# Performance work log

Hardware: AMD Instinct MI355X
Metric: run time of the kernel (lower is better)

The kernel has to match this reference:

```python
import jax, jax.numpy as jnp
import numpy as np

B, S, C, HEADS, DMODEL = 16, 14, 2048, 4, 512
C8 = C // 8
N = S * S
F = C * N  # flattened per-head feature size


def setup_inputs() -> dict:
    key = jax.random.key(0)
    ks = jax.random.split(key, 12)
    scale = 0.02
    return {
        "encoded_before_images": jax.random.normal(ks[0], (B, S, S, C), jnp.float32),
        "encoded_after_images": jax.random.normal(ks[1], (B, S, S, C), jnp.float32),
        "Wq": jax.random.normal(ks[2], (HEADS, C8, C), jnp.float32) * scale,
        "bq": jax.random.normal(ks[3], (HEADS, C8), jnp.float32) * scale,
        "Wk": jax.random.normal(ks[4], (HEADS, C8, C), jnp.float32) * scale,
        "bk": jax.random.normal(ks[5], (HEADS, C8), jnp.float32) * scale,
        "Wv": jax.random.normal(ks[6], (HEADS, C, C), jnp.float32) * scale,
        "bv": jax.random.normal(ks[7], (HEADS, C), jnp.float32) * scale,
        "gamma": jax.random.normal(ks[8], (HEADS,), jnp.float32) * 0.1,
        "Wl": jax.random.normal(ks[9], (DMODEL, F), jnp.float32) * 0.005,
        "bl": jax.random.normal(ks[10], (DMODEL,), jnp.float32) * scale,
    }


def reference(encoded_before_images, encoded_after_images,
              Wq, bq, Wk, bk, Wv, bv, gamma, Wl, bl):
    # permute to (B, C, H, W) then flatten spatial -> (B, C, N)
    before = jnp.transpose(encoded_before_images, (0, 3, 1, 2)).reshape(B, C, N)
    after = jnp.transpose(encoded_after_images, (0, 3, 1, 2)).reshape(B, C, N)
    diff = (after - before) / (HEADS - 1)
    i = jnp.arange(HEADS, dtype=before.dtype)[:, None, None, None]
    x = before[None] + i * diff[None]        # image_trajectory: (H, B, C, N)
    d = i * diff[None]                        # change_trajectory: (H, B, C, N)

    # per-head 1x1 convs (Q from image, K from change image, V from image)
    Q = jnp.einsum('hoc,hbcn->hbno', Wq, x) + bq[:, None, None, :]   # (H,B,N,C8)
    K = jnp.einsum('hoc,hbcn->hbon', Wk, d) + bk[:, None, :, None]   # (H,B,C8,N)
    energy = jnp.einsum('hbno,hbom->hbnm', Q, K)                     # (H,B,N,N)
    attn = jax.nn.softmax(energy, axis=-1)
    V = jnp.einsum('hoc,hbcn->hbon', Wv, x) + bv[:, None, :, None]   # (H,B,C,N)
    # out[b,c,m] = sum_n V[b,c,n] * attn[b,m,n]
    out = jnp.einsum('hbcn,hbmn->hbcm', V, attn)                      # (H,B,C,N)
    out = gamma[:, None, None, None] * out + x                        # residual

    # stack heads last, flatten (C,H,W), heads become "sequence" dim
    feats = jnp.transpose(out, (1, 2, 3, 0)).reshape(B, F, HEADS)     # (B, C*N, H)
    feats = jnp.transpose(feats, (0, 2, 1))                           # (B, H, F)
    output = feats @ Wl.T + bl                                        # (B, H, DMODEL)

    alphas = jax.lax.stop_gradient(jnp.transpose(attn, (1, 2, 3, 0))[:, None])  # (B,1,N,N,H)
    return (output, alphas)
```

## Files before the change

kernel.cpp:

```cpp
#include <hip/hip_runtime.h>
#include <hip/hip_bf16.h>

#define BB 16
#define NN 196
#define NP 224
#define CC 2048
#define C8 256
#define HH 4
#define DM 512
#define FF (CC*NN)

typedef unsigned short u16;
typedef signed char s8;
typedef __attribute__((ext_vector_type(4))) u16 u16x4;
typedef __attribute__((ext_vector_type(8))) u16 u16x8;
typedef __attribute__((ext_vector_type(8))) short bf16x8;
typedef __attribute__((ext_vector_type(4))) float f32x4;
typedef __attribute__((ext_vector_type(4))) int i32x4;

typedef __attribute__((address_space(1))) unsigned int as1_uint;
typedef __attribute__((address_space(3))) unsigned int as3_uint;

__device__ __forceinline__ void cp16(void* l, const void* g) {
    __builtin_amdgcn_global_load_lds((as1_uint*)g, (as3_uint*)l, 16, 0, 0);
}

__device__ __forceinline__ u16 f2bf(float f) {
    union { float f; unsigned u; } x; x.f = f;
    unsigned r = x.u + 0x7FFF + ((x.u >> 16) & 1);
    return (u16)(r >> 16);
}
__device__ __forceinline__ float bf2f(u16 u) {
    union { unsigned u; float f; } x; x.u = ((unsigned)u) << 16;
    return x.f;
}
__device__ __forceinline__ int q8i(float v, float s) {
    int q = __float2int_rn(fminf(fmaxf(v * s, -127.f), 127.f));
    return q & 255;
}
__device__ __forceinline__ int pk4(float a, float b, float c, float d, float s) {
    return q8i(a, s) | (q8i(b, s) << 8) | (q8i(c, s) << 16) | (q8i(d, s) << 24);
}

#define QX (127.0f / 6.0f)
#define QW (127.0f / 0.15f)
#define SCL ((6.0f / 127.0f) * (0.15f / 127.0f))

__global__ __launch_bounds__(256) void k_prep(const float* __restrict__ bef,
                                              const float* __restrict__ aft,
                                              u16* __restrict__ xhi, u16* __restrict__ xlo,
                                              u16* __restrict__ dhi, u16* __restrict__ dlo,
                                              s8* __restrict__ x8)
{
    const float inv3 = 1.0f / 3.0f;
    const size_t n4 = (size_t)BB * NN * CC / 4;
    const size_t stride = (size_t)gridDim.x * blockDim.x;
    for (size_t i = (size_t)blockIdx.x * blockDim.x + threadIdx.x; i < n4; i += stride) {
        float4 a = ((const float4*)aft)[i];
        float4 b = ((const float4*)bef)[i];
        float4 d;
        d.x = (a.x - b.x) * inv3; d.y = (a.y - b.y) * inv3;
        d.z = (a.z - b.z) * inv3; d.w = (a.w - b.w) * inv3;
        size_t bn = i >> 9;
        int c = (int)(i & 511) * 4;
        int b_ = (int)(bn / NN), n = (int)(bn % NN);
        size_t dof = ((size_t)b_ * NP + n) * CC + c;
        u16x4 h4, l4;
        h4.x = f2bf(d.x); l4.x = f2bf(d.x - bf2f(h4.x));
        h4.y = f2bf(d.y); l4.y = f2bf(d.y - bf2f(h4.y));
        h4.z = f2bf(d.z); l4.z = f2bf(d.z - bf2f(h4.z));
        h4.w = f2bf(d.w); l4.w = f2bf(d.w - bf2f(h4.w));
        *(u16x4*)(dhi + dof) = h4;
        *(u16x4*)(dlo + dof) = l4;
#pragma unroll
        for (int h = 0; h < HH; ++h) {
            float fh = (float)h;
            float4 x;
            x.x = b.x + fh * d.x; x.y = b.y + fh * d.y;
            x.z = b.z + fh * d.z; x.w = b.w + fh * d.w;
            size_t xof = ((size_t)(h * BB + b_) * NP + n) * CC + c;
            u16x4 xh4;
            xh4.x = f2bf(x.x); xh4.y = f2bf(x.y);
            xh4.z = f2bf(x.z); xh4.w = f2bf(x.w);
            *(u16x4*)(xhi + xof) = xh4;
            if (h != 0) {
                u16x4 xl4;
                xl4.x = f2bf(x.x - bf2f(xh4.x));
                xl4.y = f2bf(x.y - bf2f(xh4.y));
                xl4.z = f2bf(x.z - bf2f(xh4.z));
                xl4.w = f2bf(x.w - bf2f(xh4.w));
                *(u16x4*)(xlo + xof) = xl4;
            }
            *(int*)(x8 + xof) = pk4(x.x, x.y, x.z, x.w, QX);
        }
    }
    const size_t dpad = (size_t)BB * (NP - NN) * CC / 4;
    const u16x4 z4 = {0, 0, 0, 0};
    for (size_t i = (size_t)blockIdx.x * blockDim.x + threadIdx.x; i < dpad; i += stride) {
        size_t b_ = i / ((NP - NN) * CC / 4);
        size_t rem = i % ((NP - NN) * CC / 4);
        int pn = (int)(rem >> 9), c4 = (int)(rem & 511);
        size_t of = ((size_t)b_ * NP + NN + pn) * CC + c4 * 4;
        *(u16x4*)(dhi + of) = z4; *(u16x4*)(dlo + of) = z4;
    }
    const size_t xpad = (size_t)HH * BB * (NP - NN) * CC / 4;
    for (size_t i = (size_t)blockIdx.x * blockDim.x + threadIdx.x; i < xpad; i += stride) {
        size_t hb = i / ((NP - NN) * CC / 4);
        size_t rem = i % ((NP - NN) * CC / 4);
        int pn = (int)(rem >> 9), c4 = (int)(rem & 511);
        size_t of = ((size_t)hb * NP + NN + pn) * CC + c4 * 4;
        *(u16x4*)(xhi + of) = z4; *(u16x4*)(xlo + of) = z4;
        *(int*)(x8 + of) = 0;
    }
}

__global__ __launch_bounds__(256) void k_castW(const float* __restrict__ Wq,
                                               const float* __restrict__ Wk,
                                               const float* __restrict__ Wv,
                                               u16* __restrict__ wqh, u16* __restrict__ wql,
                                               u16* __restrict__ wkh, u16* __restrict__ wkl,
                                               s8* __restrict__ Wv8)
{
    const size_t qk = (size_t)HH * C8 * CC / 4;
    const size_t wv = (size_t)HH * CC * CC / 4;
    const size_t tot = qk * 2 + wv;
    const size_t stride = (size_t)gridDim.x * blockDim.x;
    for (size_t i = (size_t)blockIdx.x * blockDim.x + threadIdx.x; i < tot; i += stride) {
        if (i < qk * 2) {
            const float* src; u16* dh; u16* dl; size_t j;
            if (i < qk) { src = Wq; dh = wqh; dl = wql; j = i; }
            else        { src = Wk; dh = wkh; dl = wkl; j = i - qk; }
            float4 f = ((const float4*)src)[j];
            u16x4 h4, l4;
            h4.x = f2bf(f.x); l4.x = f2bf(f.x - bf2f(h4.x));
            h4.y = f2bf(f.y); l4.y = f2bf(f.y - bf2f(h4.y));
            h4.z = f2bf(f.z); l4.z = f2bf(f.z - bf2f(h4.z));
            h4.w = f2bf(f.w); l4.w = f2bf(f.w - bf2f(h4.w));
            ((u16x4*)dh)[j] = h4; ((u16x4*)dl)[j] = l4;
        } else {
            size_t j = i - qk * 2;
            float4 f = ((const float4*)Wv)[j];
            *(int*)(Wv8 + 4 * j) = pk4(f.x, f.y, f.z, f.w, QW);
        }
    }
}

__global__ __launch_bounds__(256, 2) void k_qkm(
    const u16* __restrict__ xhi, const u16* __restrict__ xlo,
    const u16* __restrict__ dhi, const u16* __restrict__ dlo,
    const u16* __restrict__ wqh, const u16* __restrict__ wql,
    const u16* __restrict__ wkh, const u16* __restrict__ wkl,
    const float* __restrict__ bq, const float* __restrict__ bk,
    u16* __restrict__ Qhb, u16* __restrict__ Qlb,
    u16* __restrict__ Khb, u16* __restrict__ Klb)
{
    __shared__ u16 lds[1920 * 8];
    u16* Wh = lds;
    u16* Wl_ = lds + 512 * 8;
    u16* Xh = lds + 1024 * 8;
    u16* Xl = lds + 1472 * 8;

    const int t = threadIdx.x, w = t >> 6, ln = t & 63;
    const int lg = ln >> 4, l16 = ln & 15;
    const int id = blockIdx.x;
    const int xid = id / 96, rem = id % 96;
    const int z = rem / 48, j0 = rem % 48;
    const int hb = j0 + 16, h = hb >> 4, b = hb & 15;
    const int ct = xid & 1, mt = xid >> 1;

    const u16* Ah = (z ? dhi + (size_t)b * NP * CC : xhi + (size_t)hb * NP * CC)
                    + (size_t)(mt * 112) * CC;
    const u16* Al = (z ? dlo + (size_t)b * NP * CC : xlo + (size_t)hb * NP * CC)
                    + (size_t)(mt * 112) * CC;
    const u16* Bh = (z ? wkh : wqh) + ((size_t)h * C8 + ct * 128) * CC;
    const u16* Bl = (z ? wkl : wql) + ((size_t)h * C8 + ct * 128) * CC;
    const float scale = z ? (float)h : 1.0f;
    const float* bias = (z ? bk : bq) + h * C8;
    u16* OutH = z ? Khb : Qhb;
    u16* OutL = z ? Klb : Qlb;

    f32x4 acc[2][7];
    const f32x4 zf = {0.f, 0.f, 0.f, 0.f};
#pragma unroll
    for (int i = 0; i < 2; ++i)
#pragma unroll
        for (int j = 0; j < 7; ++j) acc[i][j] = zf;

    for (int k0 = 0; k0 < CC; k0 += 32) {
#pragma unroll
        for (int it = 0; it < 2; ++it) {
            int cell = it * 256 + t;
            int g = cell >> 7, o = cell & 127;
            cp16(Wh + (size_t)cell * 8, Bh + (size_t)o * CC + k0 + 8 * g);
            cp16(Wl_ + (size_t)cell * 8, Bl + (size_t)o * CC + k0 + 8 * g);
        }
        {
            int g = t / 112, n = t % 112;
            cp16(Xh + (size_t)t * 8, Ah + (size_t)n * CC + k0 + 8 * g);
            cp16(Xl + (size_t)t * 8, Al + (size_t)n * CC + k0 + 8 * g);
            if (t < 192) {
                int cell = 256 + t;
                int g2 = cell / 112, n2 = cell % 112;
                cp16(Xh + (size_t)cell * 8, Ah + (size_t)n2 * CC + k0 + 8 * g2);
                cp16(Xl + (size_t)cell * 8, Al + (size_t)n2 * CC + k0 + 8 * g2);
            }
        }
        __syncthreads();
        bf16x8 ah[2], al[2], bh[7], bl[7];
#pragma unroll
        for (int i = 0; i < 2; ++i) {
            ah[i] = *(const bf16x8*)(Wh + (size_t)(lg * 128 + w * 32 + i * 16 + l16) * 8);
            al[i] = *(const bf16x8*)(Wl_ + (size_t)(lg * 128 + w * 32 + i * 16 + l16) * 8);
        }
#pragma unroll
        for (int j = 0; j < 7; ++j) {
            bh[j] = *(const bf16x8*)(Xh + (size_t)(lg * 112 + j * 16 + l16) * 8);
            bl[j] = *(const bf16x8*)(Xl + (size_t)(lg * 112 + j * 16 + l16) * 8);
        }
#pragma unroll
        for (int i = 0; i < 2; ++i)
#pragma unroll
            for (int j = 0; j < 7; ++j)
                acc[i][j] = __builtin_amdgcn_mfma_f32_16x16x32_bf16(ah[i], bh[j], acc[i][j], 0, 0, 0);
#pragma unroll
        for (int i = 0; i < 2; ++i)
#pragma unroll
            for (int j = 0; j < 7; ++j)
                acc[i][j] = __builtin_amdgcn_mfma_f32_16x16x32_bf16(ah[i], bl[j], acc[i][j], 0, 0, 0);
#pragma unroll
        for (int i = 0; i < 2; ++i)
#pragma unroll
            for (int j = 0; j < 7; ++j)
                acc[i][j] = __builtin_amdgcn_mfma_f32_16x16x32_bf16(al[i], bh[j], acc[i][j], 0, 0, 0);
        __syncthreads();
    }

#pragma unroll
    for (int i = 0; i < 2; ++i) {
        int ob = ct * 128 + w * 32 + i * 16 + lg * 4;
#pragma unroll
        for (int j = 0; j < 7; ++j) {
            int n = mt * 112 + j * 16 + l16;
            u16x4 hv, lv;
#pragma unroll
            for (int r = 0; r < 4; ++r) {
                float v = scale * acc[i][j][r] + bias[ob + r];
                hv[r] = f2bf(v);
                lv[r] = f2bf(v - bf2f(hv[r]));
            }
            size_t of = ((size_t)hb * NP + n) * C8 + ob;
            *(u16x4*)(OutH + of) = hv;
            *(u16x4*)(OutL + of) = lv;
        }
    }
}

__global__ __launch_bounds__(256, 2) void k_esm(
    const u16* __restrict__ Qh, const u16* __restrict__ Ql,
    const u16* __restrict__ Kh, const u16* __restrict__ Kl,
    float* __restrict__ alphas, u16* __restrict__ atnb)
{
    __shared__ u16 lds[2304 * 8];
    u16* QHs = lds;
    u16* QLs = lds + 256 * 8;
    u16* KHs = lds + 512 * 8;
    u16* KLs = lds + 1408 * 8;

    const int t = threadIdx.x, w = t >> 6, ln = t & 63;
    const int lg = ln >> 4, l16 = ln & 15;
    const int hb = blockIdx.x, mt = blockIdx.y;
    const int h = hb >> 4, b = hb & 15;

    if (h == 0) {
        const float uni = 1.0f / 196.0f;
        const u16 ub = f2bf(uni);
        for (int idx = t; idx < 64 * NP; idx += 256) {
            int m = mt * 64 + idx / NP;
            int n = idx % NP;
            if (m < NP) {
                atnb[((size_t)hb * NP + m) * NP + n] = (n < NN) ? ub : (u16)0;
                if (m < NN && n < NN)
                    alphas[(((size_t)b * NN + m) * NN + n) * HH + 0] = uni;
            }
        }
        return;
    }

    const size_t base = (size_t)hb * NP * C8;

    f32x4 e[14];
    const f32x4 zf = {0.f, 0.f, 0.f, 0.f};
#pragma unroll
    for (int j = 0; j < 14; ++j) e[j] = zf;

    for (int o0 = 0; o0 < C8; o0 += 32) {
        {
            int g = t >> 6, mr = t & 63;
            size_t src = base + (size_t)(mt * 64 + mr) * C8 + o0 + 8 * g;
            cp16(QHs + (size_t)t * 8, Qh + src);
            cp16(QLs + (size_t)t * 8, Ql + src);
        }
#pragma unroll
        for (int it = 0; it < 4; ++it) {
            int cell = it * 256 + t;
            if (cell < 896) {
                int g = cell / 224, n = cell % 224;
                size_t src = base + (size_t)n * C8 + o0 + 8 * g;
                cp16(KHs + (size_t)cell * 8, Kh + src);
                cp16(KLs + (size_t)cell * 8, Kl + src);
            }
        }
        __syncthreads();
        bf16x8 ah = *(const bf16x8*)(QHs + (size_t)(lg * 64 + w * 16 + l16) * 8);
        bf16x8 al = *(const bf16x8*)(QLs + (size_t)(lg * 64 + w * 16 + l16) * 8);
#pragma unroll
        for (int j = 0; j < 14; ++j) {
            bf16x8 bh = *(const bf16x8*)(KHs + (size_t)(lg * 224 + j * 16 + l16) * 8);
            bf16x8 bl = *(const bf16x8*)(KLs + (size_t)(lg * 224 + j * 16 + l16) * 8);
            e[j] = __builtin_amdgcn_mfma_f32_16x16x32_bf16(ah, bh, e[j], 0, 0, 0);
            e[j] = __builtin_amdgcn_mfma_f32_16x16x32_bf16(ah, bl, e[j], 0, 0, 0);
            e[j] = __builtin_amdgcn_mfma_f32_16x16x32_bf16(al, bh, e[j], 0, 0, 0);
        }
        __syncthreads();
    }

#pragma unroll
    for (int r = 0; r < 4; ++r) {
        float mx = -1e30f;
#pragma unroll
        for (int j = 0; j < 14; ++j) {
            int n = j * 16 + l16;
            if (n < NN) mx = fmaxf(mx, e[j][r]);
        }
#pragma unroll
        for (int off = 1; off <= 8; off <<= 1) mx = fmaxf(mx, __shfl_xor(mx, off));
        float p[14];
        float s = 0.f;
#pragma unroll
        for (int j = 0; j < 14; ++j) {
            int n = j * 16 + l16;
            if (n < NN) { p[j] = __expf(e[j][r] - mx); s += p[j]; }
            else p[j] = 0.f;
        }
#pragma unroll
        for (int off = 1; off <= 8; off <<= 1) s += __shfl_xor(s, off);
        const float inv = 1.0f / s;
        const int m = mt * 64 + w * 16 + lg * 4 + r;
        if (m < NP) {
            u16* arow = atnb + ((size_t)hb * NP + m) * NP;
#pragma unroll
            for (int j = 0; j < 14; ++j) {
                int n = j * 16 + l16;
                float a = p[j] * inv;
                arow[n] = f2bf(a);
                if (m < NN && n < NN)
                    alphas[(((size_t)b * NN + m) * NN + n) * HH + h] = a;
            }
        }
    }
}

__global__ __launch_bounds__(256, 2) void k_vpv(
    const s8* __restrict__ Wv8,
    const s8* __restrict__ x8,
    const u16* __restrict__ xhi,
    const u16* __restrict__ atnb,
    const float* __restrict__ bv,
    const float* __restrict__ gamma,
    u16* __restrict__ outs)
{
    __shared__ u16 lds[4992 * 8];
    s8* Aw8 = (s8*)lds;
    s8* Bx8 = (s8*)lds + 8192;
    u16* BxP = lds + 512 * 8;
    u16* Vb  = lds + 1408 * 8;

    const int t = threadIdx.x, w = t >> 6, ln = t & 63;
    const int lg = ln >> 4, l16 = ln & 15;
    const int wr = w >> 1, wc = w & 1;
    const int id = blockIdx.x;
    const int ct = id >> 6, hb = id & 63;
    const int h = hb >> 4, b = hb & 15;
    const size_t wv_base = ((size_t)h * CC + ct * 128) * CC;
    const size_t x8_base = (size_t)(h * BB + b) * NP * CC;
    const size_t xh_base = x8_base;
    const size_t p_base  = (size_t)(h * BB + b) * NP * NP;

    i32x4 acc8[4][7];
    const i32x4 zi = {0, 0, 0, 0};
#pragma unroll
    for (int i = 0; i < 4; ++i)
#pragma unroll
        for (int j = 0; j < 7; ++j) acc8[i][j] = zi;

    for (int k0 = 0; k0 < CC; k0 += 64) {
#pragma unroll
        for (int it = 0; it < 2; ++it) {
            int cell = it * 256 + t;
            int g = cell >> 7, o = cell & 127;
            cp16(Aw8 + (size_t)cell * 16, Wv8 + wv_base + (size_t)o * CC + k0 + 16 * g);
        }
#pragma unroll
        for (int it = 0; it < 4; ++it) {
            int cell = it * 256 + t;
            if (cell < 896) {
                int g = cell / NP, n = cell % NP;
                cp16(Bx8 + (size_t)cell * 16, x8 + x8_base + (size_t)n * CC + k0 + 16 * g);
            }
        }
        __syncthreads();
        i32x4 a8[4], b8[7];
#pragma unroll
        for (int i = 0; i < 4; ++i)
            a8[i] = *(const i32x4*)(Aw8 + (size_t)(lg * 128 + wr * 64 + i * 16 + l16) * 16);
#pragma unroll
        for (int j = 0; j < 7; ++j)
            b8[j] = *(const i32x4*)(Bx8 + (size_t)(lg * NP + wc * 112 + j * 16 + l16) * 16);
#pragma unroll
        for (int i = 0; i < 4; ++i)
#pragma unroll
            for (int j = 0; j < 7; ++j)
                acc8[i][j] = __builtin_amdgcn_mfma_i32_16x16x64_i8(a8[i], b8[j], acc8[i][j], 0, 0, 0);
        __syncthreads();
    }

#pragma unroll
    for (int i = 0; i < 4; ++i) {
        int cb = wr * 64 + i * 16 + lg * 4;
#pragma unroll
        for (int j = 0; j < 7; ++j) {
            int n = wc * 112 + j * 16 + l16;
#pragma unroll
            for (int r = 0; r < 4; ++r) {
                float v = (float)acc8[i][j][r] * SCL + bv[h * CC + ct * 128 + cb + r];
                Vb[(size_t)((n >> 3) * 128 + cb + r) * 8 + (n & 7)] = f2bf(v);
            }
        }
    }
    __syncthreads();

    f32x4 acc[4][7];
    const f32x4 zf = {0.f, 0.f, 0.f, 0.f};
#pragma unroll
    for (int i = 0; i < 4; ++i)
#pragma unroll
        for (int j = 0; j < 7; ++j) acc[i][j] = zf;

    for (int s = 0; s < 7; ++s) {
#pragma unroll
        for (int it = 0; it < 4; ++it) {
            if (it < 3 || w < 2) {
                int cell = it * 256 + w * 64 + ln;
                int g = cell / NP, m = cell % NP;
                cp16(BxP + (size_t)cell * 8, atnb + p_base + (size_t)m * NP + s * 32 + 8 * g);
            }
        }
        __syncthreads();
        bf16x8 a[4], bq[7];
#pragma unroll
        for (int i = 0; i < 4; ++i)
            a[i] = *(const bf16x8*)(Vb + (size_t)((4 * s + lg) * 128 + wr * 64 + i * 16 + l16) * 8);
#pragma unroll
        for (int j = 0; j < 7; ++j)
            bq[j] = *(const bf16x8*)(BxP + (size_t)(lg * NP + wc * 112 + j * 16 + l16) * 8);
#pragma unroll
        for (int i = 0; i < 4; ++i)
#pragma unroll
            for (int j = 0; j < 7; ++j)
                acc[i][j] = __builtin_amdgcn_mfma_f32_16x16x32_bf16(a[i], bq[j], acc[i][j], 0, 0, 0);
        __syncthreads();
    }

    const float gm = gamma[h];
    const size_t ob = ((size_t)(h * BB + b) * CC + ct * 128) * NN;
#pragma unroll
    for (int i = 0; i < 4; ++i) {
        int cb = wr * 64 + i * 16 + lg * 4;
#pragma unroll
        for (int j = 0; j < 7; ++j) {
            int m = wc * 112 + j * 16 + l16;
            if (m < NN) {
                const u16* xp = xhi + xh_base + (size_t)m * CC + ct * 128 + cb;
#pragma unroll
                for (int r = 0; r < 4; ++r) {
                    float ov = gm * acc[i][j][r] + bf2f(xp[r]);
                    outs[ob + (size_t)(cb + r) * NN + m] = f2bf(ov);
                }
            }
        }
    }
}

__global__ __launch_bounds__(256, 2) void k_lin(
    const u16* __restrict__ feats, const float* __restrict__ Wl,
    float* __restrict__ part)
{
    __shared__ u16 lds[(256 + 1040) * 8];
    u16* Aa = lds;
    u16* Bb = lds + 256 * 8;
    const int t = threadIdx.x, w = t >> 6, ln = t & 63;
    const int lg = ln >> 4, l16 = ln & 15;
    const int wr = w >> 1, wc = w & 1;
    const int dmt = blockIdx.x, ch = blockIdx.y;
    const int ga = t >> 6, aa = t & 63;
    const u16* asrc = feats + (size_t)((aa & 3) * BB + (aa >> 2)) * FF + (size_t)ch * 1568 + 8 * ga;
    const int fr = t & 7, rb = t >> 3;
    const int gB = fr >> 1, hB = fr & 1;
    const float* bsrc = Wl + ((size_t)dmt * 256 + rb) * FF + (size_t)ch * 1568 + fr * 4;

    f32x4 acc[2][8];
    const f32x4 zf = {0.f, 0.f, 0.f, 0.f};
#pragma unroll
    for (int i = 0; i < 2; ++i)
#pragma unroll
        for (int j = 0; j < 8; ++j) acc[i][j] = zf;

    for (int k0 = 0; k0 < 1568; k0 += 32) {
        cp16(Aa + (size_t)t * 8, asrc + k0);
#pragma unroll
        for (int rr = 0; rr < 8; ++rr) {
            int row = rr * 32 + rb;
            float4 f = *(const float4*)(bsrc + (size_t)rr * 32 * FF + k0);
            u16x4 u;
            u.x = f2bf(f.x); u.y = f2bf(f.y); u.z = f2bf(f.z); u.w = f2bf(f.w);
            *(u16x4*)(Bb + ((size_t)(gB * 260 + row)) * 8 + hB * 4) = u;
        }
        __syncthreads();
        bf16x8 a[2], bq[8];
#pragma unroll
        for (int i = 0; i < 2; ++i)
            a[i] = *(const bf16x8*)(Aa + (size_t)(lg * 64 + wr * 32 + i * 16 + l16) * 8);
#pragma unroll
        for (int j = 0; j < 8; ++j)
            bq[j] = *(const bf16x8*)(Bb + (size_t)(lg * 260 + wc * 128 + j * 16 + l16) * 8);
#pragma unroll
        for (int i = 0; i < 2; ++i)
#pragma unroll
            for (int j = 0; j < 8; ++j)
                acc[i][j] = __builtin_amdgcn_mfma_f32_16x16x32_bf16(a[i], bq[j], acc[i][j], 0, 0, 0);
        __syncthreads();
    }
#pragma unroll
    for (int i = 0; i < 2; ++i)
#pragma unroll
        for (int j = 0; j < 8; ++j)
#pragma unroll
            for (int r = 0; r < 4; ++r)
                part[((size_t)ch * 64 + wr * 32 + i * 16 + lg * 4 + r) * DM
                     + dmt * 256 + wc * 128 + j * 16 + l16] = acc[i][j][r];
}

__global__ __launch_bounds__(256) void k_red(const float* __restrict__ part,
                                             const float* __restrict__ bl,
                                             float* __restrict__ out0)
{
    int gid = blockIdx.x * 256 + threadIdx.x;
    if (gid < 64 * DM) {
        int dm = gid & (DM - 1);
        float s = bl[dm];
        for (int c2 = 0; c2 < 256; ++c2) s += part[(size_t)c2 * 64 * DM + gid];
        out0[gid] = s;
    }
}

extern "C" void kernel_launch(void* const* d_in, const int* in_sizes, int n_in,
                              void* d_out, int out_size, void* d_ws, size_t ws_size,
                              hipStream_t stream)
{
    const float* bef   = (const float*)d_in[0];
    const float* aft   = (const float*)d_in[1];
    const float* Wq    = (const float*)d_in[2];
    const float* bq    = (const float*)d_in[3];
    const float* Wk    = (const float*)d_in[4];
    const float* bk    = (const float*)d_in[5];
    const float* Wv    = (const float*)d_in[6];
    const float* bv    = (const float*)d_in[7];
    const float* gamma = (const float*)d_in[8];
    const float* Wl    = (const float*)d_in[9];
    const float* bl    = (const float*)d_in[10];

    float* out0   = (float*)d_out;
    float* alphas = out0 + (size_t)BB * HH * DM;

    float* ws = (float*)d_ws;
    u16* xhi  = (u16*)ws;
    u16* xlo  = (u16*)(ws + 14680064);
    u16* dhi  = (u16*)(ws + 29360128);
    u16* dlo  = (u16*)(ws + 33030144);
    u16* wqh  = (u16*)(ws + 36700160);
    u16* wql  = (u16*)(ws + 37748736);
    u16* wkh  = (u16*)(ws + 38797312);
    u16* wkl  = (u16*)(ws + 39845888);
    u16* Qhb  = (u16*)(ws + 40894464);
    u16* Qlb  = (u16*)(ws + 42729472);
    u16* Khb  = (u16*)(ws + 44564480);
    u16* Klb  = (u16*)(ws + 46399488);
    s8*  Wv8  = (s8*)(ws + 48234496);
    s8*  x8   = (s8*)(ws + 52428800);
    u16* atnb = (u16*)(ws + 59768832);
    u16* outs = (u16*)(ws + 61374464);
    float* part = ws + 74219520;

    k_prep<<<2048, 256, 0, stream>>>(bef, aft, xhi, xlo, dhi, dlo, x8);
    k_castW<<<2048, 256, 0, stream>>>(Wq, Wk, Wv, wqh, wql, wkh, wkl, Wv8);
    k_qkm<<<384, 256, 0, stream>>>(xhi, xlo, dhi, dlo, wqh, wql, wkh, wkl,
                                   bq, bk, Qhb, Qlb, Khb, Klb);
    k_esm<<<dim3(64, 4), 256, 0, stream>>>(Qhb, Qlb, Khb, Klb, alphas, atnb);
    k_vpv<<<1024, 256, 0, stream>>>(Wv8, x8, xhi, atnb, bv, gamma, outs);
    k_lin<<<dim3(2, 256), 256, 0, stream>>>(outs, Wl, part);
    k_red<<<128, 256, 0, stream>>>(part, bl, out0);
}
```

Baseline: 581.5 us.

## Fold weight casting into prep and overlap Wv quantization with QK GEMM

Removes the separate k_castW launch. Wq/Wk bf16 hi/lo splitting moves into k_prep, and Wv int8 quantization runs in 128 extra blocks appended to the k_qkm grid, so it overlaps with the Q/K projection GEMM. This saves one kernel launch and hides the memory-bound Wv cast behind compute. The extra blocks compete with the GEMM blocks for CU slots and bandwidth, which may slow the GEMM.

```diff
diff --git a/kernel.cpp b/kernel.cpp
--- a/kernel.cpp
+++ b/kernel.cpp
@@ -48,9 +48,13 @@
 
 __global__ __launch_bounds__(256) void k_prep(const float* __restrict__ bef,
                                               const float* __restrict__ aft,
+                                              const float* __restrict__ Wq,
+                                              const float* __restrict__ Wk,
                                               u16* __restrict__ xhi, u16* __restrict__ xlo,
                                               u16* __restrict__ dhi, u16* __restrict__ dlo,
-                                              s8* __restrict__ x8)
+                                              s8* __restrict__ x8,
+                                              u16* __restrict__ wqh, u16* __restrict__ wql,
+                                              u16* __restrict__ wkh, u16* __restrict__ wkl)
 {
     const float inv3 = 1.0f / 3.0f;
     const size_t n4 = (size_t)BB * NN * CC / 4;
@@ -112,36 +116,18 @@
         *(u16x4*)(xhi + of) = z4; *(u16x4*)(xlo + of) = z4;
         *(int*)(x8 + of) = 0;
     }
-}
-
-__global__ __launch_bounds__(256) void k_castW(const float* __restrict__ Wq,
-                                               const float* __restrict__ Wk,
-                                               const float* __restrict__ Wv,
-                                               u16* __restrict__ wqh, u16* __restrict__ wql,
-                                               u16* __restrict__ wkh, u16* __restrict__ wkl,
-                                               s8* __restrict__ Wv8)
-{
     const size_t qk = (size_t)HH * C8 * CC / 4;
-    const size_t wv = (size_t)HH * CC * CC / 4;
-    const size_t tot = qk * 2 + wv;
-    const size_t stride = (size_t)gridDim.x * blockDim.x;
-    for (size_t i = (size_t)blockIdx.x * blockDim.x + threadIdx.x; i < tot; i += stride) {
-        if (i < qk * 2) {
-            const float* src; u16* dh; u16* dl; size_t j;
-            if (i < qk) { src = Wq; dh = wqh; dl = wql; j = i; }
-            else        { src = Wk; dh = wkh; dl = wkl; j = i - qk; }
-            float4 f = ((const float4*)src)[j];
-            u16x4 h4, l4;
-            h4.x = f2bf(f.x); l4.x = f2bf(f.x - bf2f(h4.x));
-            h4.y = f2bf(f.y); l4.y = f2bf(f.y - bf2f(h4.y));
-            h4.z = f2bf(f.z); l4.z = f2bf(f.z - bf2f(h4.z));
-            h4.w = f2bf(f.w); l4.w = f2bf(f.w - bf2f(h4.w));
-            ((u16x4*)dh)[j] = h4; ((u16x4*)dl)[j] = l4;
-        } else {
-            size_t j = i - qk * 2;
-            float4 f = ((const float4*)Wv)[j];
-            *(int*)(Wv8 + 4 * j) = pk4(f.x, f.y, f.z, f.w, QW);
-        }
+    for (size_t i = (size_t)blockIdx.x * blockDim.x + threadIdx.x; i < qk * 2; i += stride) {
+        const float* src; u16* dh; u16* dl; size_t j;
+        if (i < qk) { src = Wq; dh = wqh; dl = wql; j = i; }
+        else        { src = Wk; dh = wkh; dl = wkl; j = i - qk; }
+        float4 f = ((const float4*)src)[j];
+        u16x4 h4, l4;
+        h4.x = f2bf(f.x); l4.x = f2bf(f.x - bf2f(h4.x));
+        h4.y = f2bf(f.y); l4.y = f2bf(f.y - bf2f(h4.y));
+        h4.z = f2bf(f.z); l4.z = f2bf(f.z - bf2f(h4.z));
+        h4.w = f2bf(f.w); l4.w = f2bf(f.w - bf2f(h4.w));
+        ((u16x4*)dh)[j] = h4; ((u16x4*)dl)[j] = l4;
     }
 }
 
@@ -151,6 +137,7 @@
     const u16* __restrict__ wqh, const u16* __restrict__ wql,
     const u16* __restrict__ wkh, const u16* __restrict__ wkl,
     const float* __restrict__ bq, const float* __restrict__ bk,
+    const float* __restrict__ Wv, s8* __restrict__ Wv8,
     u16* __restrict__ Qhb, u16* __restrict__ Qlb,
     u16* __restrict__ Khb, u16* __restrict__ Klb)
 {
@@ -163,6 +150,16 @@
     const int t = threadIdx.x, w = t >> 6, ln = t & 63;
     const int lg = ln >> 4, l16 = ln & 15;
     const int id = blockIdx.x;
+
+    if (id >= 384) {
+        const size_t wv4 = (size_t)HH * CC * CC / 4;
+        for (size_t i = (size_t)(id - 384) * 256 + t; i < wv4; i += 128 * 256) {
+            float4 f = ((const float4*)Wv)[i];
+            *(int*)(Wv8 + 4 * i) = pk4(f.x, f.y, f.z, f.w, QW);
+        }
+        return;
+    }
+
     const int xid = id / 96, rem = id % 96;
     const int z = rem / 48, j0 = rem % 48;
     const int hb = j0 + 16, h = hb >> 4, b = hb & 15;
@@ -601,10 +598,10 @@
     u16* outs = (u16*)(ws + 61374464);
     float* part = ws + 74219520;
 
-    k_prep<<<2048, 256, 0, stream>>>(bef, aft, xhi, xlo, dhi, dlo, x8);
-    k_castW<<<2048, 256, 0, stream>>>(Wq, Wk, Wv, wqh, wql, wkh, wkl, Wv8);
-    k_qkm<<<384, 256, 0, stream>>>(xhi, xlo, dhi, dlo, wqh, wql, wkh, wkl,
-                                   bq, bk, Qhb, Qlb, Khb, Klb);
+    k_prep<<<2048, 256, 0, stream>>>(bef, aft, Wq, Wk, xhi, xlo, dhi, dlo, x8,
+                                     wqh, wql, wkh, wkl);
+    k_qkm<<<512, 256, 0, stream>>>(xhi, xlo, dhi, dlo, wqh, wql, wkh, wkl,
+                                   bq, bk, Wv, Wv8, Qhb, Qlb, Khb, Klb);
     k_esm<<<dim3(64, 4), 256, 0, stream>>>(Qhb, Qlb, Khb, Klb, alphas, atnb);
     k_vpv<<<1024, 256, 0, stream>>>(Wv8, x8, xhi, atnb, bv, gamma, outs);
     k_lin<<<dim3(2, 256), 256, 0, stream>>>(outs, Wl, part);
```

Result: faster. 563.0 us (median of 2 runs) (-3.2%).
